# Kernel tuning notes

Measured on AMD Instinct MI355X. Metric: run time of the kernel, lower is better.

## Reference

```python
import jax, jax.numpy as jnp
import numpy as np

FEAT_DIM = 512
NUM_CLASS = 100000
N = 512
M = 0.5
S = 64.0
COS_M = float(np.cos(M))
SIN_M = float(np.sin(M))
THRESHOLD = float(np.cos(np.pi - M))
MM = float(np.sin(np.pi - M) * M)
LABEL_SMOOTH = 0.1


def setup_inputs() -> dict:
    key = jax.random.key(0)
    k1, k2, k3 = jax.random.split(key, 3)
    embbedings = jax.random.normal(k1, (N, FEAT_DIM), dtype=jnp.float32)
    label = jax.random.randint(k2, (N,), 0, NUM_CLASS, dtype=jnp.int64 if jax.config.jax_enable_x64 else jnp.int32)
    w = 0.01 * jax.random.normal(k3, (FEAT_DIM, NUM_CLASS), dtype=jnp.float32)
    return {"embbedings": embbedings, "w": w, "label": label}


def reference(embbedings, w, label):
    n = embbedings.shape[0]
    rows = jnp.arange(n)

    # weight column-normalize (done with no_grad in torch) and feature row-normalize
    wn = w / jnp.linalg.norm(w, axis=0, keepdims=True)
    e = embbedings / jnp.linalg.norm(embbedings, axis=1, keepdims=True)

    cos_theta = jnp.clip(e @ wn, -1.0, 1.0)          # [N, C]
    target_logit = cos_theta[rows, label][:, None]    # [N, 1]

    sin_theta = jnp.sqrt(1.0 - target_logit ** 2)
    cos_theta_m = target_logit * COS_M - sin_theta * SIN_M  # cos(theta + m)

    mask = cos_theta > cos_theta_m                    # hard examples
    final_target_logit = jnp.where(target_logit > THRESHOLD,
                                   cos_theta_m, target_logit - MM)

    # adaptive t (running buffer starts at 0 -> single-step value), no grad in torch
    t = jax.lax.stop_gradient(0.01 * jnp.mean(target_logit))

    cos_theta = jnp.where(mask, cos_theta * (t + cos_theta), cos_theta)
    cos_theta = cos_theta.at[rows, label].set(final_target_logit[:, 0])

    logits = cos_theta * S
    logp = jax.nn.log_softmax(logits, axis=-1)
    nll = -logp[rows, label]
    smooth = -jnp.mean(logp, axis=-1)  # eps/C * sum_c(-logp) == eps * mean(-logp)
    loss = jnp.mean((1.0 - LABEL_SMOOTH) * nll + LABEL_SMOOTH * smooth)
    return loss
```

## Files before the change

kernel.cpp:

```cpp
#include <hip/hip_runtime.h>

#define KD    512
#define NCLS  100000
#define BC    64
#define NB    ((NCLS + BC - 1) / BC)
#define NTILE 1564
#define CPAD  100096
#define R1B   64
#define R1C   25
#define S_SCALE 64.0f
#define COS_M   0.87758256189037276f
#define SIN_M   0.47942553860420301f
#define THRESH (-0.87758256189037276f)
#define MM_C    0.23971276930210151f

typedef __attribute__((ext_vector_type(8))) short short8;
typedef __attribute__((ext_vector_type(4))) float f32x4;

union Pack8 { unsigned short u[8]; uint4 v; };

__device__ __forceinline__ unsigned short f2bf(float x) {
  unsigned int u = __float_as_uint(x);
  u += 0x7fffu + ((u >> 16) & 1u);
  return (unsigned short)(u >> 16);
}

__global__ void k0_norm(const float* __restrict__ emb,
                        unsigned short* __restrict__ eb, float* __restrict__ rnA) {
  int r = blockIdx.x;
  int l = threadIdx.x;
  const float* src = emb + (size_t)r * KD + l * 8;
  float v[8];
  float ss = 0.f;
#pragma unroll
  for (int j = 0; j < 8; ++j) { v[j] = src[j]; ss += v[j] * v[j]; }
#pragma unroll
  for (int m = 1; m < 64; m <<= 1) ss += __shfl_xor(ss, m, 64);
  float rn = rsqrtf(ss);
  Pack8 p;
#pragma unroll
  for (int j = 0; j < 8; ++j) p.u[j] = f2bf(v[j] * rn);
  *reinterpret_cast<uint4*>(eb + (size_t)r * KD + l * 8) = p.v;
  if (l == 0) rnA[r] = rn;
}

__global__ __launch_bounds__(512)
void k_tgt(const float* __restrict__ emb, const float* __restrict__ w,
           const int* __restrict__ label, float2* __restrict__ tpart) {
  const int j = blockIdx.x;
  const int r = threadIdx.x;
  const int lab = label[r];
  const float* wc = w + lab;
  const float* er = emb + (size_t)r * KD + j * 8;
  float dot = 0.f, sq = 0.f;
#pragma unroll
  for (int kk = 0; kk < 8; ++kk) {
    float wv = wc[(size_t)(j * 8 + kk) * NCLS];
    float ev = er[kk];
    dot += ev * wv;
    sq  += wv * wv;
  }
  tpart[(size_t)j * 512 + r] = make_float2(dot, sq);
}

__global__ void k_prep2(const float2* __restrict__ tpart, const float* __restrict__ rnA,
                        float* __restrict__ ctmA, float* __restrict__ finA,
                        float* __restrict__ tval) {
  __shared__ float red[512];
  const int r = threadIdx.x;
  float dot = 0.f, sq = 0.f;
#pragma unroll 8
  for (int j = 0; j < 64; ++j) {
    float2 p = tpart[(size_t)j * 512 + r];
    dot += p.x; sq += p.y;
  }
  float tl = dot * rnA[r] * rsqrtf(sq);
  tl = fminf(1.f, fmaxf(-1.f, tl));
  red[r] = tl;
  __syncthreads();
  for (int s = 256; s > 0; s >>= 1) {
    if (r < s) red[r] += red[r + s];
    __syncthreads();
  }
  float st = sqrtf(fmaxf(0.f, 1.f - tl * tl));
  float ctm = tl * COS_M - st * SIN_M;
  ctmA[r] = ctm;
  finA[r] = (tl > THRESH) ? ctm : (tl - MM_C);
  if (r == 0) tval[0] = 0.01f * red[0] * (1.f / 512.f);
}

__global__ __launch_bounds__(1024)
void k_w(const float* __restrict__ w, unsigned short* __restrict__ wb,
         float* __restrict__ sqpart) {
  const int tid = threadIdx.x;
  const int ch  = blockIdx.x >> 2;
  const int kh  = blockIdx.x & 3;
  const int c   = ch * 1024 + tid;
  const int cc  = (c < NCLS) ? c : (NCLS - 1);
  const bool valid = (c < NCLS);
  const bool wvalid = (c < CPAD);
  const int cb = c >> 6;
  const int ct = (c >> 4) & 3;
  const int cl = c & 15;
  unsigned short* gdst = wb + (size_t)cb * 32768 + ct * 128 + cl * 8;
  const float* srcc = w + cc;
  float sq = 0.f;
#pragma unroll 2
  for (int o16 = 0; o16 < 16; ++o16) {
    const int o = kh * 16 + o16;
    float v[8];
#pragma unroll
    for (int j = 0; j < 8; ++j)
      v[j] = __builtin_nontemporal_load(&srcc[(size_t)(o * 8 + j) * NCLS]);
    Pack8 p;
#pragma unroll
    for (int j = 0; j < 8; ++j) {
      float x = valid ? v[j] : 0.f;
      sq += x * x;
      p.u[j] = f2bf(x);
    }
    if (wvalid) *reinterpret_cast<uint4*>(gdst + (size_t)o * 512) = p.v;
  }
  if (wvalid) sqpart[(size_t)kh * CPAD + c] = sq;
}

__global__ __launch_bounds__(512, 4)
void k_gemm(const unsigned short* __restrict__ wb, const float* __restrict__ sqpart,
            const unsigned short* __restrict__ eb,
            const int* __restrict__ label, const float* __restrict__ ctmA,
            const float* __restrict__ finA, const float* __restrict__ tval,
            float2* __restrict__ part) {
  __shared__ float invnS[BC];
  __shared__ float sE[512];
  __shared__ float sL[512];
  const int tid = threadIdx.x;
  const int wv = tid >> 6;
  const int l  = tid & 63;
  const int c0 = blockIdx.x * BC;

  if (tid < BC) {
    const int c = c0 + tid;
    float s = sqpart[0 * (size_t)CPAD + c] + sqpart[1 * (size_t)CPAD + c]
            + sqpart[2 * (size_t)CPAD + c] + sqpart[3 * (size_t)CPAD + c];
    invnS[tid] = (s > 0.f) ? rsqrtf(s) : 0.f;
  }
  __syncthreads();

  const int q  = l >> 4;
  const int cl = l & 15;
  const int rbase = wv * 64;
  const unsigned short* bt = wb + (size_t)blockIdx.x * 32768 + q * 512 + cl * 8;
  f32x4 acc[4][4] = {};

#pragma unroll 1
  for (int s = 0; s < 16; ++s) {
    const int k0 = s * 32 + q * 8;
    short8 a[4], b[4];
#pragma unroll
    for (int ct = 0; ct < 4; ++ct)
      b[ct] = *reinterpret_cast<const short8*>(bt + s * 2048 + ct * 128);
#pragma unroll
    for (int rt = 0; rt < 4; ++rt) {
      int row = rbase + rt * 16 + cl;
      a[rt] = *reinterpret_cast<const short8*>(eb + (size_t)row * KD + k0);
    }
#pragma unroll
    for (int rt = 0; rt < 4; ++rt)
#pragma unroll
      for (int ct = 0; ct < 4; ++ct)
        acc[rt][ct] = __builtin_amdgcn_mfma_f32_16x16x32_bf16(a[rt], b[ct], acc[rt][ct], 0, 0, 0);
  }

  const float t = tval[0];
#pragma unroll
  for (int rt = 0; rt < 4; ++rt) {
#pragma unroll
    for (int rg = 0; rg < 4; ++rg) {
      const int row = rbase + rt * 16 + q * 4 + rg;
      const float ctm = ctmA[row];
      const float fin = finA[row];
      const int   lab = label[row];
      float se = 0.f, sl = 0.f;
#pragma unroll
      for (int ct = 0; ct < 4; ++ct) {
        const int cg = c0 + ct * 16 + cl;
        if (cg < NCLS) {
          float cosv = acc[rt][ct][rg] * invnS[ct * 16 + cl];
          cosv = fminf(1.f, fmaxf(-1.f, cosv));
          float logit = (cosv > ctm) ? cosv * (t + cosv) : cosv;
          if (cg == lab) logit = fin;
          float x = S_SCALE * logit;
          se += __expf(x);
          sl += x;
        }
      }
#pragma unroll
      for (int m = 1; m < 16; m <<= 1) {
        se += __shfl_xor(se, m, 64);
        sl += __shfl_xor(sl, m, 64);
      }
      if (cl == 0) { sE[row] = se; sL[row] = sl; }
    }
  }
  __syncthreads();

  part[(size_t)blockIdx.x * 512 + tid] = make_float2(sE[tid], sL[tid]);
}

__global__ void k0_norm_target_legacy(const float* __restrict__ emb, const float* __restrict__ w,
                               const int* __restrict__ label,
                               unsigned short* __restrict__ eb, float* __restrict__ tlA) {
  int r = blockIdx.x;
  int l = threadIdx.x;
  const float* src = emb + (size_t)r * KD + l * 8;
  float v[8];
  float ss = 0.f;
#pragma unroll
  for (int j = 0; j < 8; ++j) { v[j] = src[j]; ss += v[j] * v[j]; }
#pragma unroll
  for (int m = 1; m < 64; m <<= 1) ss += __shfl_xor(ss, m, 64);
  float rn = rsqrtf(ss);
  Pack8 p;
#pragma unroll
  for (int j = 0; j < 8; ++j) {
    float x = v[j] * rn;
    v[j] = x;
    p.u[j] = f2bf(x);
  }
  *reinterpret_cast<uint4*>(eb + (size_t)r * KD + l * 8) = p.v;
  int lab = label[r];
  float wv[8];
#pragma unroll
  for (int j = 0; j < 8; ++j) wv[j] = w[(size_t)(l * 8 + j) * NCLS + lab];
  float dot = 0.f, sq = 0.f;
#pragma unroll
  for (int j = 0; j < 8; ++j) { dot += v[j] * wv[j]; sq += wv[j] * wv[j]; }
#pragma unroll
  for (int m = 1; m < 64; m <<= 1) {
    dot += __shfl_xor(dot, m, 64);
    sq  += __shfl_xor(sq, m, 64);
  }
  if (l == 0) {
    float tl = dot * rsqrtf(sq);
    tlA[r] = fminf(1.f, fmaxf(-1.f, tl));
  }
}

__global__ void k_prep(const float* __restrict__ tlA, float* __restrict__ ctmA,
                       float* __restrict__ finA, float* __restrict__ tval) {
  __shared__ float red[512];
  int i = threadIdx.x;
  float tl = tlA[i];
  red[i] = tl;
  __syncthreads();
  for (int s = 256; s > 0; s >>= 1) {
    if (i < s) red[i] += red[i + s];
    __syncthreads();
  }
  float st = sqrtf(fmaxf(0.f, 1.f - tl * tl));
  float ctm = tl * COS_M - st * SIN_M;
  ctmA[i] = ctm;
  finA[i] = (tl > THRESH) ? ctm : (tl - MM_C);
  if (i == 0) tval[0] = 0.01f * red[0] * (1.f / 512.f);
}

__global__ __launch_bounds__(256, 2)
void k_gemm_legacy(const float* __restrict__ w, const unsigned short* __restrict__ eb,
            const int* __restrict__ label, const float* __restrict__ ctmA,
            const float* __restrict__ finA, const float* __restrict__ tval,
            float2* __restrict__ part) {
  __shared__ __align__(16) unsigned short Bs[BC * KD];
  __shared__ float ssW[4][BC];
  __shared__ float invnS[BC];
  __shared__ float sE[512];
  __shared__ float sL[512];
  const int tid = threadIdx.x;
  const int wv = tid >> 6;
  const int l  = tid & 63;
  const int c0 = blockIdx.x * BC;
  {
    const int c = l;
    const int cgc = (c0 + c < NCLS) ? (c0 + c) : (NCLS - 1);
    const float* wp = w + cgc;
    float ss = 0.f;
#pragma unroll 1
    for (int ph = 0; ph < 2; ++ph) {
      float vb[8][8];
#pragma unroll
      for (int b = 0; b < 8; ++b) {
        const int kb = wv * 8 + (ph * 8 + b) * 32;
#pragma unroll
        for (int j = 0; j < 8; ++j)
          vb[b][j] = __builtin_nontemporal_load(&wp[(size_t)(kb + j) * NCLS]);
      }
      __builtin_amdgcn_sched_barrier(0);
#pragma unroll
      for (int b = 0; b < 8; ++b) {
        const int kb = wv * 8 + (ph * 8 + b) * 32;
        Pack8 p;
#pragma unroll
        for (int j = 0; j < 8; ++j) {
          float x = vb[b][j];
          ss += x * x;
          p.u[j] = f2bf(x);
        }
        const int G = c * 64 + ((kb >> 3) ^ (c & 7));
        *reinterpret_cast<uint4*>(&Bs[G * 8]) = p.v;
      }
    }
    ssW[wv][c] = ss;
  }
  __syncthreads();
  if (tid < BC) {
    float s = ssW[0][tid] + ssW[1][tid] + ssW[2][tid] + ssW[3][tid];
    invnS[tid] = (s > 0.f) ? rsqrtf(s) : 0.f;
  }
  __syncthreads();
  const int q  = l >> 4;
  const int cl = l & 15;
  const int rbase = wv * 128;
  f32x4 acc[8][4] = {};
#pragma unroll 1
  for (int s = 0; s < 16; ++s) {
    const int k0 = s * 32 + q * 8;
    short8 a[8], b[4];
#pragma unroll
    for (int ct = 0; ct < 4; ++ct) {
      int c = ct * 16 + cl;
      int G = c * 64 + ((k0 >> 3) ^ (c & 7));
      b[ct] = *reinterpret_cast<const short8*>(&Bs[G * 8]);
    }
#pragma unroll
    for (int rt = 0; rt < 8; ++rt) {
      int row = rbase + rt * 16 + cl;
      a[rt] = *reinterpret_cast<const short8*>(eb + (size_t)row * KD + k0);
    }
#pragma unroll
    for (int rt = 0; rt < 8; ++rt)
#pragma unroll
      for (int ct = 0; ct < 4; ++ct)
        acc[rt][ct] = __builtin_amdgcn_mfma_f32_16x16x32_bf16(a[rt], b[ct], acc[rt][ct], 0, 0, 0);
  }
  const float t = tval[0];
#pragma unroll
  for (int rt = 0; rt < 8; ++rt) {
#pragma unroll
    for (int rg = 0; rg < 4; ++rg) {
      const int row = rbase + rt * 16 + q * 4 + rg;
      const float ctm = ctmA[row];
      const float fin = finA[row];
      const int   lab = label[row];
      float se = 0.f, sl = 0.f;
#pragma unroll
      for (int ct = 0; ct < 4; ++ct) {
        const int cg = c0 + ct * 16 + cl;
        if (cg < NCLS) {
          float cosv = acc[rt][ct][rg] * invnS[ct * 16 + cl];
          cosv = fminf(1.f, fmaxf(-1.f, cosv));
          float logit = (cosv > ctm) ? cosv * (t + cosv) : cosv;
          if (cg == lab) logit = fin;
          float x = S_SCALE * logit;
          se += __expf(x);
          sl += x;
        }
      }
#pragma unroll
      for (int m = 1; m < 16; m <<= 1) {
        se += __shfl_xor(se, m, 64);
        sl += __shfl_xor(sl, m, 64);
      }
      if (cl == 0) { sE[row] = se; sL[row] = sl; }
    }
  }
  __syncthreads();
  {
    float2* dst = part + (size_t)blockIdx.x * 512;
    dst[tid]       = make_float2(sE[tid],       sL[tid]);
    dst[tid + 256] = make_float2(sE[tid + 256], sL[tid + 256]);
  }
}

__global__ void k_reduce1(const float2* __restrict__ part, float2* __restrict__ part2) {
  const int j = blockIdx.x;
  const int r = threadIdx.x;
  const int i0 = j * R1C;
  const int i1 = (i0 + R1C < NB) ? (i0 + R1C) : NB;
  float se = 0.f, sl = 0.f;
  for (int i = i0; i < i1; ++i) {
    float2 p = part[(size_t)i * 512 + r];
    se += p.x; sl += p.y;
  }
  part2[(size_t)j * 512 + r] = make_float2(se, sl);
}

__global__ void k_loss(const float2* __restrict__ part2, const float* __restrict__ finA,
                       float* __restrict__ out) {
  __shared__ float red[512];
  const int r = threadIdx.x;
  float se = 0.f, sl = 0.f;
#pragma unroll 4
  for (int j = 0; j < R1B; ++j) {
    float2 p = part2[(size_t)j * 512 + r];
    se += p.x; sl += p.y;
  }
  float lse = logf(se);
  float nll = lse - S_SCALE * finA[r];
  float sm  = lse - sl * (1.f / (float)NCLS);
  red[r] = 0.9f * nll + 0.1f * sm;
  __syncthreads();
  for (int s = 256; s > 0; s >>= 1) {
    if (r < s) red[r] += red[r + s];
    __syncthreads();
  }
  if (r == 0) out[0] = red[0] * (1.f / 512.f);
}

extern "C" void kernel_launch(void* const* d_in, const int* in_sizes, int n_in,
                              void* d_out, int out_size, void* d_ws, size_t ws_size,
                              hipStream_t stream) {
  (void)in_sizes; (void)n_in; (void)out_size;
  const float* emb = (const float*)d_in[0];
  const float* w   = (const float*)d_in[1];
  const int*   lab = (const int*)d_in[2];
  float* out = (float*)d_out;

  char* ws = (char*)d_ws;
  unsigned short* eb = (unsigned short*)ws;
  float* tlA   = (float*)(ws + 524288);
  float* ctmA  = tlA  + 512;
  float* finA  = ctmA + 512;
  float* tval  = finA + 512;
  float2* part  = (float2*)(ws + 524288 + 8192);
  float2* part2 = part + (size_t)NB * 512;
  const size_t wb_off = 7196672;
  unsigned short* wb = (unsigned short*)(ws + wb_off);
  float* sqpart = (float*)(ws + wb_off + (size_t)NTILE * 65536);
  const size_t need = wb_off + (size_t)NTILE * 65536 + (size_t)4 * CPAD * 4;
  float*  rnA   = (float*)part;
  float2* tpart = (float2*)((char*)part + 2048);

  if (ws_size >= need) {
    hipLaunchKernelGGL(k_w,     dim3(392), dim3(1024), 0, stream, w, wb, sqpart);
    hipLaunchKernelGGL(k0_norm, dim3(512), dim3(64),   0, stream, emb, eb, rnA);
    hipLaunchKernelGGL(k_tgt,   dim3(64),  dim3(512),  0, stream, emb, w, lab, tpart);
    hipLaunchKernelGGL(k_prep2, dim3(1),   dim3(512),  0, stream, tpart, rnA, ctmA, finA, tval);
    hipLaunchKernelGGL(k_gemm,  dim3(NB),  dim3(512),  0, stream,
                       wb, sqpart, eb, lab, ctmA, finA, tval, part);
  } else {
    hipLaunchKernelGGL(k0_norm_target_legacy, dim3(512), dim3(64), 0, stream, emb, w, lab, eb, tlA);
    hipLaunchKernelGGL(k_prep, dim3(1), dim3(512), 0, stream, tlA, ctmA, finA, tval);
    hipLaunchKernelGGL(k_gemm_legacy, dim3(NB), dim3(256), 0, stream,
                       w, eb, lab, ctmA, finA, tval, part);
  }
  hipLaunchKernelGGL(k_reduce1, dim3(R1B), dim3(512), 0, stream, part, part2);
  hipLaunchKernelGGL(k_loss,    dim3(1),   dim3(512), 0, stream, part2, finA, out);
}
```

Before: 469.2 us.

## Store operands in MFMA fragment order and stage weight tile in LDS

```diff
diff --git a/kernel.cpp b/kernel.cpp
--- a/kernel.cpp
+++ b/kernel.cpp
@@ -26,7 +26,7 @@
 }
 
 __global__ void k0_norm(const float* __restrict__ emb,
-                        unsigned short* __restrict__ eb, float* __restrict__ rnA) {
+                        unsigned short* __restrict__ ebF, float* __restrict__ rnA) {
   int r = blockIdx.x;
   int l = threadIdx.x;
   const float* src = emb + (size_t)r * KD + l * 8;
@@ -40,7 +40,8 @@
   Pack8 p;
 #pragma unroll
   for (int j = 0; j < 8; ++j) p.u[j] = f2bf(v[j] * rn);
-  *reinterpret_cast<uint4*>(eb + (size_t)r * KD + l * 8) = p.v;
+  const size_t off = (size_t)(r >> 4) * 8192 + (l >> 2) * 512 + (l & 3) * 128 + (r & 15) * 8;
+  *reinterpret_cast<uint4*>(ebF + off) = p.v;
   if (l == 0) rnA[r] = rn;
 }
 
@@ -102,7 +103,7 @@
   const int cb = c >> 6;
   const int ct = (c >> 4) & 3;
   const int cl = c & 15;
-  unsigned short* gdst = wb + (size_t)cb * 32768 + ct * 128 + cl * 8;
+  unsigned short* gdst = wb + (size_t)cb * 32768 + ct * 512 + cl * 8;
   const float* srcc = w + cc;
   float sq = 0.f;
 #pragma unroll 2
@@ -119,17 +120,19 @@
       sq += x * x;
       p.u[j] = f2bf(x);
     }
-    if (wvalid) *reinterpret_cast<uint4*>(gdst + (size_t)o * 512) = p.v;
+    if (wvalid)
+      *reinterpret_cast<uint4*>(gdst + (size_t)(o >> 2) * 2048 + (o & 3) * 128) = p.v;
   }
   if (wvalid) sqpart[(size_t)kh * CPAD + c] = sq;
 }
 
 __global__ __launch_bounds__(512, 4)
 void k_gemm(const unsigned short* __restrict__ wb, const float* __restrict__ sqpart,
-            const unsigned short* __restrict__ eb,
+            const unsigned short* __restrict__ ebF,
             const int* __restrict__ label, const float* __restrict__ ctmA,
             const float* __restrict__ finA, const float* __restrict__ tval,
             float2* __restrict__ part) {
+  __shared__ __align__(16) unsigned short Bs[BC * KD];
   __shared__ float invnS[BC];
   __shared__ float sE[512];
   __shared__ float sL[512];
@@ -138,6 +141,16 @@
   const int l  = tid & 63;
   const int c0 = blockIdx.x * BC;
 
+  {
+    const unsigned short* gsrc = wb + (size_t)blockIdx.x * 32768;
+    uint4 st[8];
+#pragma unroll
+    for (int i = 0; i < 8; ++i)
+      st[i] = *reinterpret_cast<const uint4*>(gsrc + (size_t)i * 4096 + tid * 8);
+#pragma unroll
+    for (int i = 0; i < 8; ++i)
+      *reinterpret_cast<uint4*>(Bs + (size_t)i * 4096 + tid * 8) = st[i];
+  }
   if (tid < BC) {
     const int c = c0 + tid;
     float s = sqpart[0 * (size_t)CPAD + c] + sqpart[1 * (size_t)CPAD + c]
@@ -149,21 +162,19 @@
   const int q  = l >> 4;
   const int cl = l & 15;
   const int rbase = wv * 64;
-  const unsigned short* bt = wb + (size_t)blockIdx.x * 32768 + q * 512 + cl * 8;
+  const unsigned short* at = ebF + (size_t)(wv * 4) * 8192 + l * 8;
+  const unsigned short* btl = Bs + l * 8;
   f32x4 acc[4][4] = {};
 
 #pragma unroll 1
   for (int s = 0; s < 16; ++s) {
-    const int k0 = s * 32 + q * 8;
     short8 a[4], b[4];
 #pragma unroll
     for (int ct = 0; ct < 4; ++ct)
-      b[ct] = *reinterpret_cast<const short8*>(bt + s * 2048 + ct * 128);
-#pragma unroll
-    for (int rt = 0; rt < 4; ++rt) {
-      int row = rbase + rt * 16 + cl;
-      a[rt] = *reinterpret_cast<const short8*>(eb + (size_t)row * KD + k0);
-    }
+      b[ct] = *reinterpret_cast<const short8*>(btl + s * 2048 + ct * 512);
+#pragma unroll
+    for (int rt = 0; rt < 4; ++rt)
+      a[rt] = *reinterpret_cast<const short8*>(at + (size_t)rt * 8192 + s * 512);
 #pragma unroll
     for (int rt = 0; rt < 4; ++rt)
 #pragma unroll
```

Result: faster. 418.1 us (-10.9%).
